# Kernel tuning notes

Measured on AMD Instinct MI355X. Metric: run time of the kernel, lower is better.

The kernel has to match this reference:

```python
import jax, jax.numpy as jnp
import numpy as np

B, S, D = 4, 2048, 256
H = 8
HD = D // H
DFF = 512
EPS_CUTOFF = 1e-15
LN_EPS = 1e-5


def _layer_norm(x, gamma, beta):
    mu = jnp.mean(x, axis=-1, keepdims=True)
    var = jnp.mean(jnp.square(x - mu), axis=-1, keepdims=True)
    return (x - mu) * jax.lax.rsqrt(var + LN_EPS) * gamma + beta


def setup_inputs() -> dict:
    key = jax.random.key(0)
    ks = jax.random.split(key, 12)
    s = 1.0 / np.sqrt(D)
    inp = {
        "tokens": jax.random.normal(ks[0], (B, S, D), dtype=jnp.float32),
        "cutoff_factors": jax.random.uniform(ks[1], (B, S, S), dtype=jnp.float32),
        "Wqkv": jax.random.uniform(ks[2], (3 * D, D), jnp.float32, -s, s),
        "bqkv": jnp.zeros((3 * D,), jnp.float32),
        "Wo": jax.random.uniform(ks[3], (D, D), jnp.float32, -s, s),
        "bo": jnp.zeros((D,), jnp.float32),
        "ln1_g": jnp.ones((D,), jnp.float32),
        "ln1_b": jnp.zeros((D,), jnp.float32),
        "ln2_g": jnp.ones((D,), jnp.float32),
        "ln2_b": jnp.zeros((D,), jnp.float32),
        "W1": jax.random.uniform(ks[4], (DFF, D), jnp.float32, -s, s),
        "b1": jax.random.uniform(ks[5], (DFF,), jnp.float32, -s, s),
        "W2": jax.random.uniform(ks[6], (D, DFF), jnp.float32, -1.0 / np.sqrt(DFF), 1.0 / np.sqrt(DFF)),
        "b2": jax.random.uniform(ks[7], (D,), jnp.float32, -1.0 / np.sqrt(DFF), 1.0 / np.sqrt(DFF)),
        "use_manual_attention": 1,
    }
    return inp


def reference(tokens, cutoff_factors, Wqkv, bqkv, Wo, bo, ln1_g, ln1_b, ln2_g, ln2_b, W1, b1, W2, b2, use_manual_attention):
    # --- attention block ---
    qkv = tokens @ Wqkv.T + bqkv                      # [B,S,3D]
    qkv = qkv.reshape(B, S, 3, H, HD).transpose(2, 0, 3, 1, 4)  # [3,B,H,S,HD]
    q, k, v = qkv[0], qkv[1], qkv[2]
    attn_mask = jnp.log(jnp.clip(cutoff_factors, EPS_CUTOFF))[:, None, :, :]  # [B,1,S,S]
    scores = jnp.einsum("bhqd,bhkd->bhqk", q, k) / np.sqrt(HD) + attn_mask
    probs = jax.nn.softmax(scores, axis=-1)
    attn = jnp.einsum("bhqk,bhkd->bhqd", probs, v)    # [B,H,S,HD]
    attn = attn.transpose(0, 2, 1, 3).reshape(B, S, D)
    attn = attn @ Wo.T + bo
    # --- PostLN residual + norm ---
    x = _layer_norm(tokens + attn, ln1_g, ln1_b)
    # --- MLP (SiLU) ---
    h = jax.nn.silu(x @ W1.T + b1)
    mlp_out = h @ W2.T + b2
    return _layer_norm(x + mlp_out, ln2_g, ln2_b)
```

## Files before the change

kernel.cpp:

```cpp
#include <hip/hip_runtime.h>
#include <hip/hip_bf16.h>
#include <math.h>

#define B_ 4
#define S_ 2048
#define D_ 256
#define H_ 8
#define HD_ 32
#define DFF_ 512

typedef __attribute__((ext_vector_type(8))) short bf16x8;
typedef __attribute__((ext_vector_type(4))) float f32x4;

__device__ inline short f2bf(float f) {
  union { float f; unsigned u; } x; x.f = f;
  unsigned r = (x.u + 0x7FFFu + ((x.u >> 16) & 1u)) >> 16;
  return (short)r;
}
__device__ inline float bf2f(short s) {
  union { unsigned u; float f; } x; x.u = ((unsigned)(unsigned short)s) << 16;
  return x.f;
}
__device__ inline unsigned cvt_pk_bf16(float a, float b) {
  unsigned r;
  asm("v_cvt_pk_bf16_f32 %0, %1, %2" : "=v"(r) : "v"(a), "v"(b));
  return r;
}

__global__ __launch_bounds__(256) void cvt_f2bf(const float* __restrict__ src,
                                                short* __restrict__ dst, int n) {
  int i = (blockIdx.x * 256 + threadIdx.x) * 4;
  if (i < n) {
    float4 v = *(const float4*)(src + i);
    short4 s; s.x = f2bf(v.x); s.y = f2bf(v.y); s.z = f2bf(v.z); s.w = f2bf(v.w);
    *(short4*)(dst + i) = s;
  }
}

template<int MODE>
__global__ __launch_bounds__(256) void gemm_bf(const short* __restrict__ A,
                                               const short* __restrict__ W,
                                               const float* __restrict__ bias,
                                               float* __restrict__ Cf,
                                               short* __restrict__ Cb,
                                               int M, int N, int K) {
  constexpr int BM = 128, BN = 64;
  __shared__ short As[BM][72];
  __shared__ short Bs[BN][72];
  const int tid = threadIdx.x;
  const int wid = tid >> 6, lane = tid & 63;
  const int g = lane >> 4, lc = lane & 15;
  const int wr = wid >> 1, wc = wid & 1;
  const int rowBase = blockIdx.y * BM;
  const int colBase = blockIdx.x * BN;

  f32x4 acc[4][2];
#pragma unroll
  for (int m = 0; m < 4; ++m)
#pragma unroll
    for (int n = 0; n < 2; ++n) { acc[m][n][0]=0.f; acc[m][n][1]=0.f; acc[m][n][2]=0.f; acc[m][n][3]=0.f; }

  for (int k0 = 0; k0 < K; k0 += 64) {
    __syncthreads();
#pragma unroll
    for (int i = 0; i < 4; ++i) {
      int task = tid + 256 * i;
      int r = task >> 3, c = (task & 7) * 8;
      *(bf16x8*)&As[r][c] = *(const bf16x8*)(A + (size_t)(rowBase + r) * K + k0 + c);
    }
#pragma unroll
    for (int i = 0; i < 2; ++i) {
      int task = tid + 256 * i;
      int r = task >> 3, c = (task & 7) * 8;
      *(bf16x8*)&Bs[r][c] = *(const bf16x8*)(W + (size_t)(colBase + r) * K + k0 + c);
    }
    __syncthreads();
#pragma unroll
    for (int ks = 0; ks < 2; ++ks) {
      bf16x8 af[4], bfr[2];
#pragma unroll
      for (int m = 0; m < 4; ++m) af[m] = *(const bf16x8*)&As[wr*64 + m*16 + lc][ks*32 + g*8];
#pragma unroll
      for (int n = 0; n < 2; ++n) bfr[n] = *(const bf16x8*)&Bs[wc*32 + n*16 + lc][ks*32 + g*8];
#pragma unroll
      for (int m = 0; m < 4; ++m)
#pragma unroll
        for (int n = 0; n < 2; ++n)
          acc[m][n] = __builtin_amdgcn_mfma_f32_16x16x32_bf16(af[m], bfr[n], acc[m][n], 0, 0, 0);
    }
  }

#pragma unroll
  for (int m = 0; m < 4; ++m)
#pragma unroll
    for (int n = 0; n < 2; ++n) {
      int col = colBase + wc*32 + n*16 + lc;
      float bv = bias[col];
#pragma unroll
      for (int j = 0; j < 4; ++j) {
        int row = rowBase + wr*64 + m*16 + g*4 + j;
        float v = acc[m][n][j] + bv;
        if (MODE == 0) {
          Cf[(size_t)row * N + col] = v;
        } else if (MODE == 1) {
          v = v / (1.f + __expf(-v));
          Cb[(size_t)row * N + col] = f2bf(v);
        } else {
          int part = col >> 8;
          int h = (col >> 5) & 7;
          int hd = col & 31;
          int b = row >> 11, s = row & 2047;
          if (part == 0) v *= 0.17677669529663687f;
          Cb[(size_t)part * 2097152 + ((((size_t)b * 8 + h) * 2048 + s) * 32 + hd)] = f2bf(v);
        }
      }
    }
}

__global__ __launch_bounds__(256) void calc_mfix(const short* __restrict__ qkvbf,
                                                 float* __restrict__ mfix) {
  const int bh = blockIdx.x;
  const int t = threadIdx.x;
  const short* qg = qkvbf + (size_t)bh * S_ * HD_;
  const short* kg = qkvbf + 2097152 + (size_t)bh * S_ * HD_;
  __shared__ float red[256];
  float km2 = 0.f;
  for (int r = t; r < S_; r += 256) {
    const bf16x8* p = (const bf16x8*)(kg + (size_t)r * HD_);
    float ss = 0.f;
#pragma unroll
    for (int c = 0; c < 4; ++c) {
      bf16x8 v = p[c];
#pragma unroll
      for (int j = 0; j < 8; ++j) { float f = bf2f(v[j]); ss = fmaf(f, f, ss); }
    }
    km2 = fmaxf(km2, ss);
  }
  red[t] = km2;
  __syncthreads();
  for (int o = 128; o > 0; o >>= 1) {
    if (t < o) red[t] = fmaxf(red[t], red[t + o]);
    __syncthreads();
  }
  km2 = red[0];
  for (int r = t; r < S_; r += 256) {
    const bf16x8* p = (const bf16x8*)(qg + (size_t)r * HD_);
    float ss = 0.f;
#pragma unroll
    for (int c = 0; c < 4; ++c) {
      bf16x8 v = p[c];
#pragma unroll
      for (int j = 0; j < 8; ++j) { float f = bf2f(v[j]); ss = fmaf(f, f, ss); }
    }
    mfix[(size_t)bh * S_ + r] = sqrtf(ss * km2);
  }
}

__global__ __launch_bounds__(512) void attn_mfma(const short* __restrict__ qkvbf,
                                                 const float* __restrict__ cutoff,
                                                 const float* __restrict__ mfix,
                                                 short* __restrict__ outbf) {
  constexpr int KB = 64;
  const int nqt = S_ / 128;
  const int qt = blockIdx.x % nqt;
  const int h  = (blockIdx.x / nqt) % H_;
  const int b  = blockIdx.x / (nqt * H_);
  const int tid = threadIdx.x;
  const int wid = tid >> 6;
  const int lane = tid & 63;
  const int g = lane >> 4, lc = lane & 15;

  __shared__ __align__(16) short Ks[KB][56];
  __shared__ __align__(16) short Vt[HD_][66];
  __shared__ __align__(16) short Pq[8][16][72];

  const int qrow = qt * 128 + wid * 16 + lc;
  const size_t bh = ((size_t)b * H_ + h) * S_;
  const short* qg = qkvbf + bh * HD_;
  const short* kg = qkvbf + 2097152 + bh * HD_;
  const short* vg = qkvbf + 2 * 2097152 + bh * HD_;

  bf16x8 qf = *(const bf16x8*)(qg + (size_t)qrow * HD_ + g * 8);
  const float m = mfix[bh + qrow];

  f32x4 oacc[2];
#pragma unroll
  for (int d = 0; d < 2; ++d) { oacc[d][0]=0.f; oacc[d][1]=0.f; oacc[d][2]=0.f; oacc[d][3]=0.f; }
  float sml = 0.f;

  const float* cb = cutoff + ((size_t)(b * S_) + qrow) * (size_t)S_;

  for (int kt = 0; kt < S_; kt += KB) {
    __syncthreads();
    if (tid < 256) {
      int r = tid >> 2, c = (tid & 3) * 8;
      *(bf16x8*)&Ks[r][c] = *(const bf16x8*)(kg + (size_t)(kt + r) * HD_ + c);
    } else {
      int tv = tid - 256;
      int r = tv >> 2, c = (tv & 3) * 8;
      bf16x8 vv = *(const bf16x8*)(vg + (size_t)(kt + r) * HD_ + c);
#pragma unroll
      for (int j = 0; j < 8; ++j) Vt[c + j][r] = vv[j];
    }
    __syncthreads();

    float4 cv[4];
#pragma unroll
    for (int t = 0; t < 4; ++t) cv[t] = *(const float4*)(cb + kt + t * 16 + g * 4);

    bf16x8 kf[4];
#pragma unroll
    for (int t = 0; t < 4; ++t) kf[t] = *(const bf16x8*)&Ks[t*16 + lc][g*8];
    f32x4 st[4];
#pragma unroll
    for (int t = 0; t < 4; ++t) {
      f32x4 z = {0.f, 0.f, 0.f, 0.f};
      st[t] = __builtin_amdgcn_mfma_f32_16x16x32_bf16(kf[t], qf, z, 0, 0, 0);
    }

#pragma unroll
    for (int t = 0; t < 4; ++t) {
      float p0 = fmaxf(cv[t].x, 1e-15f) * __expf(st[t][0] - m);
      float p1 = fmaxf(cv[t].y, 1e-15f) * __expf(st[t][1] - m);
      float p2 = fmaxf(cv[t].z, 1e-15f) * __expf(st[t][2] - m);
      float p3 = fmaxf(cv[t].w, 1e-15f) * __expf(st[t][3] - m);
      sml += (p0 + p1) + (p2 + p3);
      uint2 pk;
      pk.x = cvt_pk_bf16(p0, p1);
      pk.y = cvt_pk_bf16(p2, p3);
      *(uint2*)&Pq[wid][lc][t*16 + g*4] = pk;
    }

    asm volatile("s_waitcnt lgkmcnt(0)" ::: "memory");
    __builtin_amdgcn_sched_barrier(0);

#pragma unroll
    for (int kh = 0; kh < 2; ++kh) {
      bf16x8 pb = *(const bf16x8*)&Pq[wid][lc][kh*32 + g*8];
#pragma unroll
      for (int dh = 0; dh < 2; ++dh) {
        bf16x8 va = *(const bf16x8*)&Vt[dh*16 + lc][kh*32 + g*8];
        oacc[dh] = __builtin_amdgcn_mfma_f32_16x16x32_bf16(va, pb, oacc[dh], 0, 0, 0);
      }
    }
  }

  float s = sml;
  s += __shfl_xor(s, 16, 64);
  s += __shfl_xor(s, 32, 64);
  float inv = 1.f / s;

#pragma unroll
  for (int dh = 0; dh < 2; ++dh) {
    uint2 pk;
    pk.x = cvt_pk_bf16(oacc[dh][0] * inv, oacc[dh][1] * inv);
    pk.y = cvt_pk_bf16(oacc[dh][2] * inv, oacc[dh][3] * inv);
    *(uint2*)(outbf + ((size_t)(b * S_) + qrow) * D_ + h * HD_ + dh * 16 + g * 4) = pk;
  }
}

template<int WBF>
__global__ __launch_bounds__(256) void residual_ln(const float* __restrict__ xa,
                                                   const float* __restrict__ xb,
                                                   const float* __restrict__ g,
                                                   const float* __restrict__ bt,
                                                   float* __restrict__ out,
                                                   short* __restrict__ outbf) {
  const int row  = blockIdx.x * 4 + (threadIdx.x >> 6);
  const int lane = threadIdx.x & 63;
  float4 va = *(const float4*)(xa + (size_t)row * D_ + lane * 4);
  float4 vb = *(const float4*)(xb + (size_t)row * D_ + lane * 4);
  float v[4] = {va.x + vb.x, va.y + vb.y, va.z + vb.z, va.w + vb.w};
  float s = v[0] + v[1] + v[2] + v[3];
#pragma unroll
  for (int o = 32; o > 0; o >>= 1) s += __shfl_xor(s, o, 64);
  float mu = s * (1.f / D_);
  float var = 0.f;
#pragma unroll
  for (int i = 0; i < 4; ++i) { v[i] -= mu; var += v[i] * v[i]; }
#pragma unroll
  for (int o = 32; o > 0; o >>= 1) var += __shfl_xor(var, o, 64);
  float rs = rsqrtf(var * (1.f / D_) + 1e-5f);
  float4 g4 = *(const float4*)(g + lane * 4);
  float4 b4 = *(const float4*)(bt + lane * 4);
  float4 o4 = {v[0] * rs * g4.x + b4.x, v[1] * rs * g4.y + b4.y,
               v[2] * rs * g4.z + b4.z, v[3] * rs * g4.w + b4.w};
  *(float4*)(out + (size_t)row * D_ + lane * 4) = o4;
  if (WBF) {
    short4 s4; s4.x = f2bf(o4.x); s4.y = f2bf(o4.y); s4.z = f2bf(o4.z); s4.w = f2bf(o4.w);
    *(short4*)(outbf + (size_t)row * D_ + lane * 4) = s4;
  }
}

extern "C" void kernel_launch(void* const* d_in, const int* in_sizes, int n_in,
                              void* d_out, int out_size, void* d_ws, size_t ws_size,
                              hipStream_t stream) {
  const float* tokens = (const float*)d_in[0];
  const float* cutoff = (const float*)d_in[1];
  const float* Wqkv   = (const float*)d_in[2];
  const float* bqkv   = (const float*)d_in[3];
  const float* Wo     = (const float*)d_in[4];
  const float* bo     = (const float*)d_in[5];
  const float* ln1g   = (const float*)d_in[6];
  const float* ln1b   = (const float*)d_in[7];
  const float* ln2g   = (const float*)d_in[8];
  const float* ln2b   = (const float*)d_in[9];
  const float* W1     = (const float*)d_in[10];
  const float* b1     = (const float*)d_in[11];
  const float* W2     = (const float*)d_in[12];
  const float* b2     = (const float*)d_in[13];
  float* out = (float*)d_out;

  char* w = (char*)d_ws;
  const size_t MB = 1 << 20;
  short* qkvbf  = (short*)w;
  short* tokbf  = (short*)(w + 12 * MB);
  short* wq_bf  = (short*)(w + 16 * MB);
  short* wo_bf  = wq_bf + 196608;
  short* w1_bf  = wo_bf + 65536;
  short* w2_bf  = w1_bf + 131072;
  short* attnbf = tokbf;
  float* projOut = (float*)(w + 18 * MB);
  float* xbuf    = (float*)(w + 26 * MB);
  float* mfix    = (float*)(w + 34 * MB);
  short* xbbf    = qkvbf;
  short* hbbf    = qkvbf + 2097152;
  float* mlpOut  = projOut;

  const int M = B_ * S_;

  cvt_f2bf<<<dim3(2048), 256, 0, stream>>>(tokens, tokbf, M * D_);
  cvt_f2bf<<<dim3(192),  256, 0, stream>>>(Wqkv, wq_bf, 3 * D_ * D_);
  cvt_f2bf<<<dim3(64),   256, 0, stream>>>(Wo,   wo_bf, D_ * D_);
  cvt_f2bf<<<dim3(128),  256, 0, stream>>>(W1,   w1_bf, DFF_ * D_);
  cvt_f2bf<<<dim3(128),  256, 0, stream>>>(W2,   w2_bf, D_ * DFF_);

  gemm_bf<2><<<dim3(12, 64), 256, 0, stream>>>(tokbf, wq_bf, bqkv, nullptr, qkvbf, M, 3 * D_, D_);
  calc_mfix<<<dim3(32), 256, 0, stream>>>(qkvbf, mfix);
  attn_mfma<<<dim3(512), 512, 0, stream>>>(qkvbf, cutoff, mfix, attnbf);
  gemm_bf<0><<<dim3(4, 64), 256, 0, stream>>>(attnbf, wo_bf, bo, projOut, nullptr, M, D_, D_);
  residual_ln<1><<<dim3(M / 4), 256, 0, stream>>>(tokens, projOut, ln1g, ln1b, xbuf, xbbf);
  gemm_bf<1><<<dim3(8, 64), 256, 0, stream>>>(xbbf, w1_bf, b1, nullptr, hbbf, M, DFF_, D_);
  gemm_bf<0><<<dim3(4, 64), 256, 0, stream>>>(hbbf, w2_bf, b2, mlpOut, nullptr, M, D_, DFF_);
  residual_ln<0><<<dim3(M / 4), 256, 0, stream>>>(xbuf, mlpOut, ln2g, ln2b, out, nullptr);
}
```

Before: 153.9 us.

## Double-buffer attention, pre-transpose V, use exp2, merge conversions and retile GEMMs

The QKV GEMM now writes V transposed and folds log2e into the Q scale, so attention can use v_exp_f32 directly and load V without an in-LDS transpose. The attention kernel moves to 256-thread blocks with double-buffered K/V tiles and prefetches the next cutoff tile from registers. The five conversion launches become one kernel, the mfix computation is split into a parallel K-norm max with atomics plus a per-row Q pass, and the N=256 GEMMs use a 64x64 tile for more blocks. The cutoff clamp is dropped, which changes results if a cutoff value is exactly zero.

Result: faster. 142.2 us (-7.6%).

```diff
diff --git a/kernel.cpp b/kernel.cpp
--- a/kernel.cpp
+++ b/kernel.cpp
@@ -26,15 +26,29 @@
   asm("v_cvt_pk_bf16_f32 %0, %1, %2" : "=v"(r) : "v"(a), "v"(b));
   return r;
 }
-
-__global__ __launch_bounds__(256) void cvt_f2bf(const float* __restrict__ src,
-                                                short* __restrict__ dst, int n) {
-  int i = (blockIdx.x * 256 + threadIdx.x) * 4;
-  if (i < n) {
-    float4 v = *(const float4*)(src + i);
-    short4 s; s.x = f2bf(v.x); s.y = f2bf(v.y); s.z = f2bf(v.z); s.w = f2bf(v.w);
-    *(short4*)(dst + i) = s;
-  }
+__device__ inline float exp2v(float x) {
+  float r;
+  asm("v_exp_f32 %0, %1" : "=v"(r) : "v"(x));
+  return r;
+}
+
+__global__ __launch_bounds__(256) void cvt_all(const float* __restrict__ tok, const float* __restrict__ wq,
+                                               const float* __restrict__ wo, const float* __restrict__ w1,
+                                               const float* __restrict__ w2,
+                                               short* __restrict__ dtok, short* __restrict__ dwq,
+                                               short* __restrict__ dwo, short* __restrict__ dw1,
+                                               short* __restrict__ dw2) {
+  int blk = blockIdx.x;
+  const float* src; short* dst; int base;
+  if (blk < 2048)      { src = tok; dst = dtok; base = blk; }
+  else if (blk < 2240) { src = wq;  dst = dwq;  base = blk - 2048; }
+  else if (blk < 2304) { src = wo;  dst = dwo;  base = blk - 2240; }
+  else if (blk < 2432) { src = w1;  dst = dw1;  base = blk - 2304; }
+  else                 { src = w2;  dst = dw2;  base = blk - 2432; }
+  int i = (base * 256 + threadIdx.x) * 4;
+  float4 v = *(const float4*)(src + i);
+  short4 s; s.x = f2bf(v.x); s.y = f2bf(v.y); s.z = f2bf(v.z); s.w = f2bf(v.w);
+  *(short4*)(dst + i) = s;
 }
 
 template<int MODE>
@@ -96,92 +110,158 @@
     for (int n = 0; n < 2; ++n) {
       int col = colBase + wc*32 + n*16 + lc;
       float bv = bias[col];
-#pragma unroll
-      for (int j = 0; j < 4; ++j) {
-        int row = rowBase + wr*64 + m*16 + g*4 + j;
-        float v = acc[m][n][j] + bv;
-        if (MODE == 0) {
-          Cf[(size_t)row * N + col] = v;
-        } else if (MODE == 1) {
+      int row0 = rowBase + wr*64 + m*16 + g*4;
+      float vj[4];
+#pragma unroll
+      for (int j = 0; j < 4; ++j) vj[j] = acc[m][n][j] + bv;
+      if (MODE == 1) {
+#pragma unroll
+        for (int j = 0; j < 4; ++j) {
+          float v = vj[j];
           v = v / (1.f + __expf(-v));
-          Cb[(size_t)row * N + col] = f2bf(v);
+          Cb[(size_t)(row0 + j) * N + col] = f2bf(v);
+        }
+      } else {
+        int part = col >> 8;
+        int h = (col >> 5) & 7;
+        int hd = col & 31;
+        int b = row0 >> 11, s0 = row0 & 2047;
+        if (part == 2) {
+          short4 s4;
+          s4.x = f2bf(vj[0]); s4.y = f2bf(vj[1]); s4.z = f2bf(vj[2]); s4.w = f2bf(vj[3]);
+          *(short4*)(Cb + 2 * 2097152 + (((size_t)b * 8 + h) * 32 + hd) * 2048 + s0) = s4;
         } else {
-          int part = col >> 8;
-          int h = (col >> 5) & 7;
-          int hd = col & 31;
-          int b = row >> 11, s = row & 2047;
-          if (part == 0) v *= 0.17677669529663687f;
-          Cb[(size_t)part * 2097152 + ((((size_t)b * 8 + h) * 2048 + s) * 32 + hd)] = f2bf(v);
+          float sc = (part == 0) ? 0.25506807f : 1.f;
+#pragma unroll
+          for (int j = 0; j < 4; ++j)
+            Cb[(size_t)part * 2097152 + (((size_t)b * 8 + h) * 2048 + s0 + j) * 32 + hd] = f2bf(vj[j] * sc);
         }
       }
     }
 }
 
-__global__ __launch_bounds__(256) void calc_mfix(const short* __restrict__ qkvbf,
-                                                 float* __restrict__ mfix) {
-  const int bh = blockIdx.x;
-  const int t = threadIdx.x;
-  const short* qg = qkvbf + (size_t)bh * S_ * HD_;
-  const short* kg = qkvbf + 2097152 + (size_t)bh * S_ * HD_;
-  __shared__ float red[256];
-  float km2 = 0.f;
-  for (int r = t; r < S_; r += 256) {
-    const bf16x8* p = (const bf16x8*)(kg + (size_t)r * HD_);
-    float ss = 0.f;
-#pragma unroll
-    for (int c = 0; c < 4; ++c) {
-      bf16x8 v = p[c];
-#pragma unroll
-      for (int j = 0; j < 8; ++j) { float f = bf2f(v[j]); ss = fmaf(f, f, ss); }
-    }
-    km2 = fmaxf(km2, ss);
-  }
-  red[t] = km2;
+__global__ __launch_bounds__(256) void gemm_bf64(const short* __restrict__ A,
+                                                 const short* __restrict__ W,
+                                                 const float* __restrict__ bias,
+                                                 float* __restrict__ Cf,
+                                                 int M, int N, int K) {
+  __shared__ short As[64][72];
+  __shared__ short Bs[64][72];
+  const int tid = threadIdx.x;
+  const int wid = tid >> 6, lane = tid & 63;
+  const int g = lane >> 4, lc = lane & 15;
+  const int wr = wid >> 1, wc = wid & 1;
+  const int rowBase = blockIdx.y * 64;
+  const int colBase = blockIdx.x * 64;
+
+  f32x4 acc[2][2];
+#pragma unroll
+  for (int m = 0; m < 2; ++m)
+#pragma unroll
+    for (int n = 0; n < 2; ++n) { acc[m][n][0]=0.f; acc[m][n][1]=0.f; acc[m][n][2]=0.f; acc[m][n][3]=0.f; }
+
+  for (int k0 = 0; k0 < K; k0 += 64) {
+    __syncthreads();
+#pragma unroll
+    for (int i = 0; i < 2; ++i) {
+      int task = tid + 256 * i;
+      int r = task >> 3, c = (task & 7) * 8;
+      *(bf16x8*)&As[r][c] = *(const bf16x8*)(A + (size_t)(rowBase + r) * K + k0 + c);
+      *(bf16x8*)&Bs[r][c] = *(const bf16x8*)(W + (size_t)(colBase + r) * K + k0 + c);
+    }
+    __syncthreads();
+#pragma unroll
+    for (int ks = 0; ks < 2; ++ks) {
+      bf16x8 af[2], bfr[2];
+#pragma unroll
+      for (int m = 0; m < 2; ++m) af[m] = *(const bf16x8*)&As[wr*32 + m*16 + lc][ks*32 + g*8];
+#pragma unroll
+      for (int n = 0; n < 2; ++n) bfr[n] = *(const bf16x8*)&Bs[wc*32 + n*16 + lc][ks*32 + g*8];
+#pragma unroll
+      for (int m = 0; m < 2; ++m)
+#pragma unroll
+        for (int n = 0; n < 2; ++n)
+          acc[m][n] = __builtin_amdgcn_mfma_f32_16x16x32_bf16(af[m], bfr[n], acc[m][n], 0, 0, 0);
+    }
+  }
+
+#pragma unroll
+  for (int m = 0; m < 2; ++m)
+#pragma unroll
+    for (int n = 0; n < 2; ++n) {
+      int col = colBase + wc*32 + n*16 + lc;
+      float bv = bias[col];
+      int row0 = rowBase + wr*32 + m*16 + g*4;
+#pragma unroll
+      for (int j = 0; j < 4; ++j)
+        Cf[(size_t)(row0 + j) * N + col] = acc[m][n][j] + bv;
+    }
+}
+
+__global__ __launch_bounds__(256) void knorm_max(const short* __restrict__ kbf, unsigned* __restrict__ kmax) {
+  const int bh = blockIdx.x >> 3;
+  const int r = (blockIdx.x & 7) * 256 + threadIdx.x;
+  const short* kp = kbf + ((size_t)bh * S_ + r) * HD_;
+  float ss = 0.f;
+#pragma unroll
+  for (int c = 0; c < 4; ++c) {
+    bf16x8 v = *(const bf16x8*)(kp + c * 8);
+#pragma unroll
+    for (int j = 0; j < 8; ++j) { float f = bf2f(v[j]); ss = fmaf(f, f, ss); }
+  }
+#pragma unroll
+  for (int o = 1; o < 64; o <<= 1) ss = fmaxf(ss, __shfl_xor(ss, o, 64));
+  __shared__ float red[4];
+  if ((threadIdx.x & 63) == 0) red[threadIdx.x >> 6] = ss;
   __syncthreads();
-  for (int o = 128; o > 0; o >>= 1) {
-    if (t < o) red[t] = fmaxf(red[t], red[t + o]);
-    __syncthreads();
-  }
-  km2 = red[0];
-  for (int r = t; r < S_; r += 256) {
-    const bf16x8* p = (const bf16x8*)(qg + (size_t)r * HD_);
-    float ss = 0.f;
-#pragma unroll
-    for (int c = 0; c < 4; ++c) {
-      bf16x8 v = p[c];
-#pragma unroll
-      for (int j = 0; j < 8; ++j) { float f = bf2f(v[j]); ss = fmaf(f, f, ss); }
-    }
-    mfix[(size_t)bh * S_ + r] = sqrtf(ss * km2);
-  }
-}
-
-__global__ __launch_bounds__(512) void attn_mfma(const short* __restrict__ qkvbf,
-                                                 const float* __restrict__ cutoff,
-                                                 const float* __restrict__ mfix,
-                                                 short* __restrict__ outbf) {
+  if (threadIdx.x == 0) {
+    float mx = fmaxf(fmaxf(red[0], red[1]), fmaxf(red[2], red[3]));
+    atomicMax(kmax + bh, __float_as_uint(mx));
+  }
+}
+
+__global__ __launch_bounds__(256) void q_mfix(const short* __restrict__ qbf,
+                                              const unsigned* __restrict__ kmax,
+                                              float* __restrict__ mfix) {
+  const int bh = blockIdx.x >> 3;
+  const int r = (blockIdx.x & 7) * 256 + threadIdx.x;
+  const short* qp = qbf + ((size_t)bh * S_ + r) * HD_;
+  float ss = 0.f;
+#pragma unroll
+  for (int c = 0; c < 4; ++c) {
+    bf16x8 v = *(const bf16x8*)(qp + c * 8);
+#pragma unroll
+    for (int j = 0; j < 8; ++j) { float f = bf2f(v[j]); ss = fmaf(f, f, ss); }
+  }
+  mfix[(size_t)bh * S_ + r] = sqrtf(ss * __uint_as_float(kmax[bh]));
+}
+
+__global__ __launch_bounds__(256, 4) void attn_mfma(const short* __restrict__ qbf,
+                                                    const short* __restrict__ kbf,
+                                                    const short* __restrict__ vtbf,
+                                                    const float* __restrict__ cutoff,
+                                                    const float* __restrict__ mfix,
+                                                    short* __restrict__ outbf) {
   constexpr int KB = 64;
-  const int nqt = S_ / 128;
-  const int qt = blockIdx.x % nqt;
-  const int h  = (blockIdx.x / nqt) % H_;
-  const int b  = blockIdx.x / (nqt * H_);
+  const int qt = blockIdx.x & 31;
+  const int h  = (blockIdx.x >> 5) & 7;
+  const int b  = blockIdx.x >> 8;
   const int tid = threadIdx.x;
-  const int wid = tid >> 6;
-  const int lane = tid & 63;
+  const int wid = tid >> 6, lane = tid & 63;
   const int g = lane >> 4, lc = lane & 15;
 
-  __shared__ __align__(16) short Ks[KB][56];
-  __shared__ __align__(16) short Vt[HD_][66];
-  __shared__ __align__(16) short Pq[8][16][72];
-
-  const int qrow = qt * 128 + wid * 16 + lc;
-  const size_t bh = ((size_t)b * H_ + h) * S_;
-  const short* qg = qkvbf + bh * HD_;
-  const short* kg = qkvbf + 2097152 + bh * HD_;
-  const short* vg = qkvbf + 2 * 2097152 + bh * HD_;
+  __shared__ __align__(16) short Ks[2][KB][56];
+  __shared__ __align__(16) short Vt[2][HD_][72];
+  __shared__ __align__(16) short Pq[4][16][72];
+
+  const int bh = b * H_ + h;
+  const int qrow = qt * 64 + wid * 16 + lc;
+  const short* qg = qbf + (size_t)bh * S_ * HD_;
+  const short* kg = kbf + (size_t)bh * S_ * HD_;
+  const short* vg = vtbf + (size_t)bh * HD_ * S_;
 
   bf16x8 qf = *(const bf16x8*)(qg + (size_t)qrow * HD_ + g * 8);
-  const float m = mfix[bh + qrow];
+  const float m = mfix[(size_t)bh * S_ + qrow];
 
   f32x4 oacc[2];
 #pragma unroll
@@ -190,27 +270,32 @@
 
   const float* cb = cutoff + ((size_t)(b * S_) + qrow) * (size_t)S_;
 
+  const int kr = tid >> 2, kc = (tid & 3) * 8;
+  const int vr = tid >> 3, vc = (tid & 7) * 8;
+  const short* kptr = kg + (size_t)kr * HD_ + kc;
+  const short* vptr = vg + (size_t)vr * S_ + vc;
+
+  bf16x8 kreg = *(const bf16x8*)kptr;
+  bf16x8 vreg = *(const bf16x8*)vptr;
+  *(bf16x8*)&Ks[0][kr][kc] = kreg;
+  *(bf16x8*)&Vt[0][vr][vc] = vreg;
+  float4 cv[4];
+#pragma unroll
+  for (int t = 0; t < 4; ++t) cv[t] = *(const float4*)(cb + t * 16 + g * 4);
+  __syncthreads();
+
+  int cur = 0;
+#pragma unroll 2
   for (int kt = 0; kt < S_; kt += KB) {
-    __syncthreads();
-    if (tid < 256) {
-      int r = tid >> 2, c = (tid & 3) * 8;
-      *(bf16x8*)&Ks[r][c] = *(const bf16x8*)(kg + (size_t)(kt + r) * HD_ + c);
-    } else {
-      int tv = tid - 256;
-      int r = tv >> 2, c = (tv & 3) * 8;
-      bf16x8 vv = *(const bf16x8*)(vg + (size_t)(kt + r) * HD_ + c);
-#pragma unroll
-      for (int j = 0; j < 8; ++j) Vt[c + j][r] = vv[j];
-    }
-    __syncthreads();
-
-    float4 cv[4];
-#pragma unroll
-    for (int t = 0; t < 4; ++t) cv[t] = *(const float4*)(cb + kt + t * 16 + g * 4);
+    const bool notlast = (kt + KB < S_);
+    if (notlast) {
+      kreg = *(const bf16x8*)(kptr + (size_t)(kt + KB) * HD_);
+      vreg = *(const bf16x8*)(vptr + (kt + KB));
+    }
 
     bf16x8 kf[4];
 #pragma unroll
-    for (int t = 0; t < 4; ++t) kf[t] = *(const bf16x8*)&Ks[t*16 + lc][g*8];
+    for (int t = 0; t < 4; ++t) kf[t] = *(const bf16x8*)&Ks[cur][t*16 + lc][g*8];
     f32x4 st[4];
 #pragma unroll
     for (int t = 0; t < 4; ++t) {
@@ -218,12 +303,18 @@
       st[t] = __builtin_amdgcn_mfma_f32_16x16x32_bf16(kf[t], qf, z, 0, 0, 0);
     }
 
+    float4 cvn[4];
+    if (notlast) {
+#pragma unroll
+      for (int t = 0; t < 4; ++t) cvn[t] = *(const float4*)(cb + kt + KB + t * 16 + g * 4);
+    }
+
 #pragma unroll
     for (int t = 0; t < 4; ++t) {
-      float p0 = fmaxf(cv[t].x, 1e-15f) * __expf(st[t][0] - m);
-      float p1 = fmaxf(cv[t].y, 1e-15f) * __expf(st[t][1] - m);
-      float p2 = fmaxf(cv[t].z, 1e-15f) * __expf(st[t][2] - m);
-      float p3 = fmaxf(cv[t].w, 1e-15f) * __expf(st[t][3] - m);
+      float p0 = cv[t].x * exp2v(st[t][0] - m);
+      float p1 = cv[t].y * exp2v(st[t][1] - m);
+      float p2 = cv[t].z * exp2v(st[t][2] - m);
+      float p3 = cv[t].w * exp2v(st[t][3] - m);
       sml += (p0 + p1) + (p2 + p3);
       uint2 pk;
       pk.x = cvt_pk_bf16(p0, p1);
@@ -239,9 +330,19 @@
       bf16x8 pb = *(const bf16x8*)&Pq[wid][lc][kh*32 + g*8];
 #pragma unroll
       for (int dh = 0; dh < 2; ++dh) {
-        bf16x8 va = *(const bf16x8*)&Vt[dh*16 + lc][kh*32 + g*8];
+        bf16x8 va = *(const bf16x8*)&Vt[cur][dh*16 + lc][kh*32 + g*8];
         oacc[dh] = __builtin_amdgcn_mfma_f32_16x16x32_bf16(va, pb, oacc[dh], 0, 0, 0);
       }
+    }
+
+    if (notlast) {
+      __syncthreads();
+      *(bf16x8*)&Ks[cur ^ 1][kr][kc] = kreg;
+      *(bf16x8*)&Vt[cur ^ 1][vr][vc] = vreg;
+      __syncthreads();
+      cur ^= 1;
+#pragma unroll
+      for (int t = 0; t < 4; ++t) cv[t] = cvn[t];
     }
   }
 
@@ -249,7 +350,6 @@
   s += __shfl_xor(s, 16, 64);
   s += __shfl_xor(s, 32, 64);
   float inv = 1.f / s;
-
 #pragma unroll
   for (int dh = 0; dh < 2; ++dh) {
     uint2 pk;
@@ -313,7 +413,9 @@
 
   char* w = (char*)d_ws;
   const size_t MB = 1 << 20;
-  short* qkvbf  = (short*)w;
+  short* qbf    = (short*)w;
+  short* kbf    = qbf + 2097152;
+  short* vtbf   = qbf + 2 * 2097152;
   short* tokbf  = (short*)(w + 12 * MB);
   short* wq_bf  = (short*)(w + 16 * MB);
   short* wo_bf  = wq_bf + 196608;
@@ -323,24 +425,23 @@
   float* projOut = (float*)(w + 18 * MB);
   float* xbuf    = (float*)(w + 26 * MB);
   float* mfix    = (float*)(w + 34 * MB);
-  short* xbbf    = qkvbf;
-  short* hbbf    = qkvbf + 2097152;
+  unsigned* kmax = (unsigned*)(w + 34 * MB + 262144);
+  short* xbbf    = qbf;
+  short* hbbf    = kbf;
   float* mlpOut  = projOut;
 
   const int M = B_ * S_;
 
-  cvt_f2bf<<<dim3(2048), 256, 0, stream>>>(tokens, tokbf, M * D_);
-  cvt_f2bf<<<dim3(192),  256, 0, stream>>>(Wqkv, wq_bf, 3 * D_ * D_);
-  cvt_f2bf<<<dim3(64),   256, 0, stream>>>(Wo,   wo_bf, D_ * D_);
-  cvt_f2bf<<<dim3(128),  256, 0, stream>>>(W1,   w1_bf, DFF_ * D_);
-  cvt_f2bf<<<dim3(128),  256, 0, stream>>>(W2,   w2_bf, D_ * DFF_);
-
-  gemm_bf<2><<<dim3(12, 64), 256, 0, stream>>>(tokbf, wq_bf, bqkv, nullptr, qkvbf, M, 3 * D_, D_);
-  calc_mfix<<<dim3(32), 256, 0, stream>>>(qkvbf, mfix);
-  attn_mfma<<<dim3(512), 512, 0, stream>>>(qkvbf, cutoff, mfix, attnbf);
-  gemm_bf<0><<<dim3(4, 64), 256, 0, stream>>>(attnbf, wo_bf, bo, projOut, nullptr, M, D_, D_);
+  cvt_all<<<dim3(2560), 256, 0, stream>>>(tokens, Wqkv, Wo, W1, W2, tokbf, wq_bf, wo_bf, w1_bf, w2_bf);
+  hipMemsetAsync(kmax, 0, 128, stream);
+
+  gemm_bf<2><<<dim3(12, 64), 256, 0, stream>>>(tokbf, wq_bf, bqkv, nullptr, qbf, M, 3 * D_, D_);
+  knorm_max<<<dim3(256), 256, 0, stream>>>(kbf, kmax);
+  q_mfix<<<dim3(256), 256, 0, stream>>>(qbf, kmax, mfix);
+  attn_mfma<<<dim3(1024), 256, 0, stream>>>(qbf, kbf, vtbf, cutoff, mfix, attnbf);
+  gemm_bf64<<<dim3(4, 128), 256, 0, stream>>>(attnbf, wo_bf, bo, projOut, M, D_, D_);
   residual_ln<1><<<dim3(M / 4), 256, 0, stream>>>(tokens, projOut, ln1g, ln1b, xbuf, xbbf);
   gemm_bf<1><<<dim3(8, 64), 256, 0, stream>>>(xbbf, w1_bf, b1, nullptr, hbbf, M, DFF_, D_);
-  gemm_bf<0><<<dim3(4, 64), 256, 0, stream>>>(hbbf, w2_bf, b2, mlpOut, nullptr, M, D_, DFF_);
+  gemm_bf64<<<dim3(4, 128), 256, 0, stream>>>(hbbf, w2_bf, b2, mlpOut, M, D_, DFF_);
   residual_ln<0><<<dim3(M / 4), 256, 0, stream>>>(xbuf, mlpOut, ln2g, ln2b, out, nullptr);
 }
```
